# Kernel tuning notes

Measured on AMD Instinct MI355X. Metric: run time of the kernel, lower is better.

## Reference

```python
import jax, jax.numpy as jnp
import numpy as np

B, S, D_MODEL = 2, 2048, 1024
HEADS = 16
DK = D_MODEL // HEADS  # 64
Q_RANK, RANK = 6, 2
ROPE_BASE = 10000.0


def _xavier(key, shape):
    # torch nn.init.xavier_uniform_ on weight (out,in); stored here as (in,out)
    fan_in, fan_out = shape
    a = (6.0 / (fan_in + fan_out)) ** 0.5
    return jax.random.uniform(key, shape, jnp.float32, -a, a)


def setup_inputs() -> dict:
    key = jax.random.key(0)
    ks = jax.random.split(key, 10)
    inp = {
        "q": jax.random.normal(ks[0], (B, S, D_MODEL), jnp.float32),
        "k": jax.random.normal(ks[1], (B, S, D_MODEL), jnp.float32),
        "v": jax.random.normal(ks[2], (B, S, D_MODEL), jnp.float32),
        # causal mask; mask==0 -> -inf in scores
        "mask": jnp.tril(jnp.ones((S, S), dtype=bool))[None, None],
        "W_Aq": _xavier(ks[3], (D_MODEL, Q_RANK * HEADS)),
        "W_Ak": _xavier(ks[4], (D_MODEL, RANK * HEADS)),
        "W_Av": _xavier(ks[5], (D_MODEL, RANK * HEADS)),
        "W_Bq": _xavier(ks[6], (D_MODEL, Q_RANK * DK)),
        "W_Bk": _xavier(ks[7], (D_MODEL, RANK * DK)),
        "W_Bv": _xavier(ks[8], (D_MODEL, RANK * DK)),
        "Wo": _xavier(ks[9], (D_MODEL, D_MODEL)),
    }
    return inp


def _rotary_cos_sin(seq_len, dim):
    inv_freq = 1.0 / (ROPE_BASE ** (jnp.arange(0, dim, 2, dtype=jnp.float32) / dim))
    freqs = jnp.outer(jnp.arange(seq_len, dtype=jnp.float32), inv_freq)  # [S, dim/2]
    return jnp.cos(freqs)[None, :, None, :], jnp.sin(freqs)[None, :, None, :]


def _apply_rotary(x, cos, sin):
    # x: [B, S, R, dk]; rotate-half style RoPE
    d = x.shape[-1] // 2
    x1, x2 = x[..., :d], x[..., d:]
    return jnp.concatenate([x1 * cos + x2 * sin, -x1 * sin + x2 * cos], axis=-1)


def reference(q, k, v, mask, W_Aq, W_Ak, W_Av, W_Bq, W_Bk, W_Bv, Wo):
    Bn, Sn, D = q.shape
    # low-rank factor projections
    A_q = (q @ W_Aq).reshape(Bn, Sn, HEADS, Q_RANK)
    A_k = (k @ W_Ak).reshape(Bn, Sn, HEADS, RANK)
    A_v = (v @ W_Av).reshape(Bn, Sn, HEADS, RANK)
    B_q = (q @ W_Bq).reshape(Bn, Sn, Q_RANK, DK)
    B_k = (k @ W_Bk).reshape(Bn, Sn, RANK, DK)
    B_v = (v @ W_Bv).reshape(Bn, Sn, RANK, DK)
    cos, sin = _rotary_cos_sin(Sn, DK)
    B_q = _apply_rotary(B_q, cos, sin)
    B_k = _apply_rotary(B_k, cos, sin)
    # reconstruct per-head q/k/v: [B,H,S,dk]
    qh = jnp.einsum("bshr,bsrd->bhsd", A_q, B_q) / Q_RANK
    kh = jnp.einsum("bshr,bsrd->bhsd", A_k, B_k) / RANK
    vh = jnp.einsum("bshr,bsrd->bhsd", A_v, B_v) / RANK
    # NOTE: original divides by d_k (not sqrt(d_k)) -- faithful to source
    score = jnp.einsum("bhqd,bhkd->bhqk", qh, kh) / DK
    score = jnp.where(mask, score, -jnp.inf)
    # dropout is identity (eval / dropout=0.0)
    att = jax.nn.softmax(score, axis=-1)
    out = jnp.einsum("bhqk,bhkd->bqhd", att, vh).reshape(Bn, Sn, D)
    return out @ Wo
```

## Files before the change

kernel.cpp:

```cpp
#include <hip/hip_runtime.h>
#include <hip/hip_bf16.h>


typedef __attribute__((ext_vector_type(8))) short short8;
typedef __attribute__((ext_vector_type(4))) float floatx4;

#define MFMA16(a, b, c) __builtin_amdgcn_mfma_f32_16x16x32_bf16(a, b, c, 0, 0, 0)

__device__ __forceinline__ float b2f(short s) {
    unsigned int u = ((unsigned int)(unsigned short)s) << 16;
    float f; __builtin_memcpy(&f, &u, 4); return f;
}
__device__ __forceinline__ unsigned short bfbits(float x) {
    __hip_bfloat16 h = __float2bfloat16(x);
    unsigned short u; __builtin_memcpy(&u, &h, 2); return u;
}

__device__ __forceinline__ float wsrc(int n, int k,
                                      const float* __restrict__ Aq, const float* __restrict__ Bq,
                                      const float* __restrict__ Ak, const float* __restrict__ Bk,
                                      const float* __restrict__ Av, const float* __restrict__ Bv,
                                      const float* __restrict__ Wo) {
    if (n < 96) return Aq[(size_t)k * 96 + n];
    if (n < 480) return Bq[(size_t)k * 384 + (n - 96)];
    if (n < 512) return 0.f;
    if (n < 544) return Ak[(size_t)k * 32 + (n - 512)];
    if (n < 672) return Bk[(size_t)k * 128 + (n - 544)];
    if (n < 768) return 0.f;
    if (n < 800) return Av[(size_t)k * 32 + (n - 768)];
    if (n < 928) return Bv[(size_t)k * 128 + (n - 800)];
    if (n < 1024) return 0.f;
    return Wo[(size_t)k * 1024 + (n - 1024)];
}

__global__ __launch_bounds__(256) void pack_wT_kernel(const float* __restrict__ Aq,
                                                      const float* __restrict__ Bq,
                                                      const float* __restrict__ Ak,
                                                      const float* __restrict__ Bk,
                                                      const float* __restrict__ Av,
                                                      const float* __restrict__ Bv,
                                                      const float* __restrict__ Wo,
                                                      __hip_bfloat16* __restrict__ outBase) {
    __shared__ float tile[64][65];
    int k0 = blockIdx.x * 64, n0 = blockIdx.y * 64;
    int tid = threadIdx.x;
#pragma unroll
    for (int p = 0; p < 16; ++p) {
        int idx = p * 256 + tid;
        int kl = idx >> 6, nl = idx & 63;
        tile[kl][nl] = wsrc(n0 + nl, k0 + kl, Aq, Bq, Ak, Bk, Av, Bv, Wo);
    }
    __syncthreads();
#pragma unroll
    for (int p = 0; p < 16; ++p) {
        int idx = p * 256 + tid;
        int nl = idx >> 6, kl = idx & 63;
        outBase[(size_t)(n0 + nl) * 1024 + k0 + kl] = __float2bfloat16(tile[kl][nl]);
    }
}

__global__ __launch_bounds__(256) void gemm3_kernel(const float* __restrict__ q,
                                                    const float* __restrict__ k,
                                                    const float* __restrict__ v,
                                                    const __hip_bfloat16* __restrict__ WT,
                                                    __hip_bfloat16* __restrict__ Pq,
                                                    __hip_bfloat16* __restrict__ Pk,
                                                    __hip_bfloat16* __restrict__ Pv) {
    __shared__ __align__(16) __hip_bfloat16 As[64][72];
    __shared__ __align__(16) __hip_bfloat16 Bs[128][72];
    int lin = blockIdx.x;
    int t = (lin >> 3) & 7;
    int mi = (lin & 7) + ((lin >> 6) << 3);
    int m0 = mi * 64;
    const float* A; __hip_bfloat16* C; int N, n0, wrow;
    if (t < 4)      { A = q; C = Pq; N = 512; n0 = t * 128;        wrow = t * 128; }
    else if (t < 6) { A = k; C = Pk; N = 256; n0 = (t - 4) * 128;  wrow = 512 + (t - 4) * 128; }
    else            { A = v; C = Pv; N = 256; n0 = (t - 6) * 128;  wrow = 768 + (t - 6) * 128; }
    int tid = threadIdx.x;
    int wave = tid >> 6, lane = tid & 63, quad = lane >> 4, l15 = lane & 15;
    floatx4 acc[4][2];
#pragma unroll
    for (int mt = 0; mt < 4; ++mt)
#pragma unroll
        for (int nt = 0; nt < 2; ++nt) acc[mt][nt] = (floatx4){0.f, 0.f, 0.f, 0.f};

    for (int k0 = 0; k0 < 1024; k0 += 64) {
#pragma unroll
        for (int pp = 0; pp < 4; ++pp) {
            int idx = pp * 256 + tid;
            int row = idx >> 4, c4 = (idx & 15) * 4;
            float4 av = *(const float4*)(A + (size_t)(m0 + row) * 1024 + k0 + c4);
            ushort4 bv;
            bv.x = bfbits(av.x); bv.y = bfbits(av.y); bv.z = bfbits(av.z); bv.w = bfbits(av.w);
            *(ushort4*)&As[row][c4] = bv;
        }
#pragma unroll
        for (int pp = 0; pp < 4; ++pp) {
            int idx = pp * 256 + tid;
            int row = idx >> 3, c8 = (idx & 7) * 8;
            *(uint4*)&Bs[row][c8] = *(const uint4*)(WT + (size_t)(wrow + row) * 1024 + k0 + c8);
        }
        __syncthreads();
#pragma unroll
        for (int ks = 0; ks < 64; ks += 32) {
            short8 af[4], bf[2];
#pragma unroll
            for (int mt = 0; mt < 4; ++mt)
                af[mt] = *(const short8*)&As[mt * 16 + l15][ks + quad * 8];
#pragma unroll
            for (int nt = 0; nt < 2; ++nt)
                bf[nt] = *(const short8*)&Bs[wave * 32 + nt * 16 + l15][ks + quad * 8];
#pragma unroll
            for (int mt = 0; mt < 4; ++mt)
#pragma unroll
                for (int nt = 0; nt < 2; ++nt)
                    acc[mt][nt] = MFMA16(af[mt], bf[nt], acc[mt][nt]);
        }
        __syncthreads();
    }
#pragma unroll
    for (int mt = 0; mt < 4; ++mt)
#pragma unroll
        for (int nt = 0; nt < 2; ++nt)
#pragma unroll
            for (int r = 0; r < 4; ++r) {
                int row = m0 + mt * 16 + quad * 4 + r;
                int col = n0 + wave * 32 + nt * 16 + l15;
                C[(size_t)row * N + col] = __float2bfloat16(acc[mt][nt][r]);
            }
}

__global__ __launch_bounds__(256) void gemm_out_kernel(const __hip_bfloat16* __restrict__ A,
                                                       const __hip_bfloat16* __restrict__ BT,
                                                       float* __restrict__ C) {
    __shared__ __align__(16) __hip_bfloat16 As[64][72];
    __shared__ __align__(16) __hip_bfloat16 Bs[128][72];
    int lin = blockIdx.x;
    int n0 = ((lin >> 3) & 7) * 128;
    int mi = (lin & 7) + ((lin >> 6) << 3);
    int m0 = mi * 64;
    int tid = threadIdx.x;
    int wave = tid >> 6, lane = tid & 63, quad = lane >> 4, l15 = lane & 15;
    floatx4 acc[4][2];
#pragma unroll
    for (int mt = 0; mt < 4; ++mt)
#pragma unroll
        for (int nt = 0; nt < 2; ++nt) acc[mt][nt] = (floatx4){0.f, 0.f, 0.f, 0.f};

    for (int k0 = 0; k0 < 1024; k0 += 64) {
#pragma unroll
        for (int pp = 0; pp < 2; ++pp) {
            int idx = pp * 256 + tid;
            int row = idx >> 3, c8 = (idx & 7) * 8;
            *(uint4*)&As[row][c8] = *(const uint4*)(A + (size_t)(m0 + row) * 1024 + k0 + c8);
        }
#pragma unroll
        for (int pp = 0; pp < 4; ++pp) {
            int idx = pp * 256 + tid;
            int row = idx >> 3, c8 = (idx & 7) * 8;
            *(uint4*)&Bs[row][c8] = *(const uint4*)(BT + (size_t)(n0 + row) * 1024 + k0 + c8);
        }
        __syncthreads();
#pragma unroll
        for (int ks = 0; ks < 64; ks += 32) {
            short8 af[4], bf[2];
#pragma unroll
            for (int mt = 0; mt < 4; ++mt)
                af[mt] = *(const short8*)&As[mt * 16 + l15][ks + quad * 8];
#pragma unroll
            for (int nt = 0; nt < 2; ++nt)
                bf[nt] = *(const short8*)&Bs[wave * 32 + nt * 16 + l15][ks + quad * 8];
#pragma unroll
            for (int mt = 0; mt < 4; ++mt)
#pragma unroll
                for (int nt = 0; nt < 2; ++nt)
                    acc[mt][nt] = MFMA16(af[mt], bf[nt], acc[mt][nt]);
        }
        __syncthreads();
    }
#pragma unroll
    for (int mt = 0; mt < 4; ++mt)
#pragma unroll
        for (int nt = 0; nt < 2; ++nt)
#pragma unroll
            for (int r = 0; r < 4; ++r) {
                int row = m0 + mt * 16 + quad * 4 + r;
                int col = n0 + wave * 32 + nt * 16 + l15;
                C[(size_t)row * 1024 + col] = acc[mt][nt][r];
            }
}

__global__ __launch_bounds__(256) void combine_vt_kernel(const __hip_bfloat16* __restrict__ Pq,
                                                         const __hip_bfloat16* __restrict__ Pk,
                                                         const __hip_bfloat16* __restrict__ Pv,
                                                         __hip_bfloat16* __restrict__ qh,
                                                         __hip_bfloat16* __restrict__ kh,
                                                         __hip_bfloat16* __restrict__ vT) {
    __shared__ __align__(16) __hip_bfloat16 LAq[16][96];
    __shared__ __align__(16) __hip_bfloat16 LAk[16][32];
    __shared__ __align__(16) __hip_bfloat16 LAv[16][32];
    __shared__ __align__(16) __hip_bfloat16 LBq[16][6][72];
    __shared__ __align__(16) __hip_bfloat16 LBk[16][2][72];
    __shared__ __align__(16) __hip_bfloat16 LBv[16][2][72];
    int tid = threadIdx.x;
    int token0 = blockIdx.x * 16;
    int b = token0 >> 11, s0 = token0 & 2047, bh0 = b * 16;

    for (int i = tid; i < 16 * 512; i += 256) {
        int s = i >> 9, c = i & 511;
        __hip_bfloat16 val = Pq[(size_t)(token0 + s) * 512 + c];
        if (c < 96) LAq[s][c] = val;
        else if (c < 480) LBq[s][(c - 96) >> 6][(c - 96) & 63] = val;
    }
    for (int i = tid; i < 16 * 256; i += 256) {
        int s = i >> 8, c = i & 255;
        __hip_bfloat16 vk = Pk[(size_t)(token0 + s) * 256 + c];
        __hip_bfloat16 vv = Pv[(size_t)(token0 + s) * 256 + c];
        if (c < 32) { LAk[s][c] = vk; LAv[s][c] = vv; }
        else if (c < 160) {
            LBk[s][(c - 32) >> 6][(c - 32) & 63] = vk;
            LBv[s][(c - 32) >> 6][(c - 32) & 63] = vv;
        }
    }
    __syncthreads();
    for (int i = tid; i < 4096; i += 256) {
        int s = i >> 8, rr = (i >> 5) & 7, d = i & 31;
        float inv = __expf(-(float)d * 0.28782313662425576f);
        float rev = (float)(s0 + s) * inv * 0.15915494309189535f;
        rev -= floorf(rev);
        float sn = __builtin_amdgcn_sinf(rev);
        float cs = __builtin_amdgcn_cosf(rev);
        if (rr < 6) {
            float x1 = b2f(*(short*)&LBq[s][rr][d]), x2 = b2f(*(short*)&LBq[s][rr][d + 32]);
            LBq[s][rr][d] = __float2bfloat16(x1 * cs + x2 * sn);
            LBq[s][rr][d + 32] = __float2bfloat16(-x1 * sn + x2 * cs);
        } else {
            int r2 = rr - 6;
            float x1 = b2f(*(short*)&LBk[s][r2][d]), x2 = b2f(*(short*)&LBk[s][r2][d + 32]);
            LBk[s][r2][d] = __float2bfloat16(x1 * cs + x2 * sn);
            LBk[s][r2][d + 32] = __float2bfloat16(-x1 * sn + x2 * cs);
        }
    }
    __syncthreads();
    const float QSCALE = 1.4426950408889634f / 768.0f;
    {
        int s = tid >> 4, h = tid & 15;
        float aq[6], ak0, ak1;
#pragma unroll
        for (int r = 0; r < 6; ++r) aq[r] = b2f(*(short*)&LAq[s][h * 6 + r]);
        ak0 = b2f(*(short*)&LAk[s][h * 2]);
        ak1 = b2f(*(short*)&LAk[s][h * 2 + 1]);
        size_t obase = ((size_t)(bh0 + h) * 2048 + s0 + s) * 64;
#pragma unroll
        for (int dc = 0; dc < 64; dc += 8) {
            float accq[8] = {0, 0, 0, 0, 0, 0, 0, 0};
#pragma unroll
            for (int r = 0; r < 6; ++r) {
                short8 bq = *(const short8*)&LBq[s][r][dc];
#pragma unroll
                for (int e = 0; e < 8; ++e) accq[e] += aq[r] * b2f(bq[e]);
            }
            short8 bk0 = *(const short8*)&LBk[s][0][dc];
            short8 bk1 = *(const short8*)&LBk[s][1][dc];
            ushort outq[8], outk[8];
#pragma unroll
            for (int e = 0; e < 8; ++e) {
                outq[e] = bfbits(accq[e] * QSCALE);
                outk[e] = bfbits(ak0 * b2f(bk0[e]) + ak1 * b2f(bk1[e]));
            }
            *(uint4*)((__hip_bfloat16*)qh + obase + dc) = *(uint4*)outq;
            *(uint4*)((__hip_bfloat16*)kh + obase + dc) = *(uint4*)outk;
        }
    }
    {
        int s = tid & 15, dg = tid >> 4;
#pragma unroll
        for (int h = 0; h < 16; ++h) {
            float a0 = b2f(*(short*)&LAv[s][h * 2]) * 0.5f;
            float a1 = b2f(*(short*)&LAv[s][h * 2 + 1]) * 0.5f;
#pragma unroll
            for (int dd = 0; dd < 4; ++dd) {
                int d = dg * 4 + dd;
                float val = a0 * b2f(*(short*)&LBv[s][0][d]) + a1 * b2f(*(short*)&LBv[s][1][d]);
                vT[((size_t)(bh0 + h) * 64 + d) * 2048 + s0 + s] = __float2bfloat16(val);
            }
        }
    }
}

__global__ __launch_bounds__(256) void flash_kernel(const __hip_bfloat16* __restrict__ qh,
                                                    const __hip_bfloat16* __restrict__ kh,
                                                    const __hip_bfloat16* __restrict__ vT,
                                                    __hip_bfloat16* __restrict__ att) {
    int lin = blockIdx.x + (blockIdx.y << 5);
    int bh = ((lin & 7) << 2) | ((lin >> 3) & 3);
    int tpair = lin >> 5;
    int tid = threadIdx.x;
    int wave = tid >> 6, lane = tid & 63, quad = lane >> 4, l15 = lane & 15;
    __shared__ __align__(16) __hip_bfloat16 Ks[64][72];
    __shared__ __align__(16) __hip_bfloat16 Vts[64][72];

    int row0 = tid >> 3, col = (tid & 7) * 8;
    int row1 = 32 + row0;
    const size_t khb = (size_t)bh * 2048 * 64;
    const size_t vtb = (size_t)bh * 64 * 2048;
    uint4 sk0, sk1, sv0, sv1;
#define FL_ISSUE(J)                                                            \
    {                                                                          \
        int k0_ = (J) * 64;                                                    \
        sk0 = *(const uint4*)(kh + khb + (size_t)(k0_ + row0) * 64 + col);     \
        sk1 = *(const uint4*)(kh + khb + (size_t)(k0_ + row1) * 64 + col);     \
        sv0 = *(const uint4*)(vT + vtb + (size_t)row0 * 2048 + k0_ + col);     \
        sv1 = *(const uint4*)(vT + vtb + (size_t)row1 * 2048 + k0_ + col);     \
    }

    for (int pass = 0; pass < 2; ++pass) {
        int qi = pass ? tpair : (31 - tpair);
        int q0 = qi * 64;
        const __hip_bfloat16* qrow =
            qh + ((size_t)bh * 2048 + q0 + wave * 16 + l15) * 64 + quad * 8;
        short8 aq0 = *(const short8*)(qrow);
        short8 aq1 = *(const short8*)(qrow + 32);

        floatx4 o[4];
#pragma unroll
        for (int nt = 0; nt < 4; ++nt) o[nt] = (floatx4){0.f, 0.f, 0.f, 0.f};
        float rs = 0.f;
        int qloc = wave * 16 + l15;

        FL_ISSUE(0);
        for (int j = 0; j <= qi; ++j) {
            __syncthreads();
            *(uint4*)&Ks[row0][col] = sk0;
            *(uint4*)&Ks[row1][col] = sk1;
            *(uint4*)&Vts[row0][col] = sv0;
            *(uint4*)&Vts[row1][col] = sv1;
            __syncthreads();
            if (j < qi) FL_ISSUE(j + 1);

            floatx4 s[4];
#pragma unroll
            for (int nt = 0; nt < 4; ++nt) s[nt] = (floatx4){0.f, 0.f, 0.f, 0.f};
#pragma unroll
            for (int nt = 0; nt < 4; ++nt) {
                short8 bk0 = *(const short8*)&Ks[nt * 16 + l15][quad * 8];
                short8 bk1 = *(const short8*)&Ks[nt * 16 + l15][32 + quad * 8];
                s[nt] = MFMA16(bk0, aq0, s[nt]);
                s[nt] = MFMA16(bk1, aq1, s[nt]);
            }
            if (j == qi) {
#pragma unroll
                for (int nt = 0; nt < 4; ++nt) {
                    int kbase = nt * 16 + quad * 4;
#pragma unroll
                    for (int r = 0; r < 4; ++r)
                        if (kbase + r > qloc) s[nt][r] = -__builtin_inff();
                }
            }
            float pv[4][4];
#pragma unroll
            for (int nt = 0; nt < 4; ++nt)
#pragma unroll
                for (int r = 0; r < 4; ++r) {
                    pv[nt][r] = exp2f(s[nt][r]);
                    rs += pv[nt][r];
                }
            union { ushort u[8]; short8 v; } p0, p1;
#pragma unroll
            for (int r = 0; r < 4; ++r) {
                p0.u[r]     = bfbits(pv[0][r]);
                p0.u[4 + r] = bfbits(pv[1][r]);
                p1.u[r]     = bfbits(pv[2][r]);
                p1.u[4 + r] = bfbits(pv[3][r]);
            }
#pragma unroll
            for (int nt = 0; nt < 4; ++nt) {
                int vr = nt * 16 + l15;
                union { ushort4 h[2]; short8 v; } x0, x1;
                x0.h[0] = *(const ushort4*)&Vts[vr][quad * 4];
                x0.h[1] = *(const ushort4*)&Vts[vr][16 + quad * 4];
                x1.h[0] = *(const ushort4*)&Vts[vr][32 + quad * 4];
                x1.h[1] = *(const ushort4*)&Vts[vr][48 + quad * 4];
                o[nt] = MFMA16(x0.v, p0.v, o[nt]);
                o[nt] = MFMA16(x1.v, p1.v, o[nt]);
            }
        }
        rs += __shfl_xor(rs, 16, 64);
        rs += __shfl_xor(rs, 32, 64);
        float inv = 1.0f / rs;
        int b = bh >> 4, h = bh & 15;
        size_t obase = ((size_t)b * 2048 + q0 + wave * 16 + l15) * 1024 + h * 64 + quad * 4;
#pragma unroll
        for (int nt = 0; nt < 4; ++nt) {
            ushort ow[4];
#pragma unroll
            for (int r = 0; r < 4; ++r) ow[r] = bfbits(o[nt][r] * inv);
            *(ushort4*)((__hip_bfloat16*)att + obase + nt * 16) = *(ushort4*)ow;
        }
    }
#undef FL_ISSUE
}

extern "C" void kernel_launch(void* const* d_in, const int* in_sizes, int n_in,
                              void* d_out, int out_size, void* d_ws, size_t ws_size,
                              hipStream_t stream) {
    const float* q = (const float*)d_in[0];
    const float* k = (const float*)d_in[1];
    const float* v = (const float*)d_in[2];
    const float* W_Aq = (const float*)d_in[4];
    const float* W_Ak = (const float*)d_in[5];
    const float* W_Av = (const float*)d_in[6];
    const float* W_Bq = (const float*)d_in[7];
    const float* W_Bk = (const float*)d_in[8];
    const float* W_Bv = (const float*)d_in[9];
    const float* Wo = (const float*)d_in[10];
    float* out = (float*)d_out;

    char* w = (char*)d_ws;
    __hip_bfloat16* qh  = (__hip_bfloat16*)(w + 0);
    __hip_bfloat16* kh  = (__hip_bfloat16*)(w + 8388608);
    __hip_bfloat16* vT  = (__hip_bfloat16*)(w + 16777216);
    __hip_bfloat16* WT  = (__hip_bfloat16*)(w + 25165824);
    __hip_bfloat16* WoT = WT + (size_t)1024 * 1024;
    __hip_bfloat16* Pq  = (__hip_bfloat16*)(w + 29360128);
    __hip_bfloat16* Pk  = (__hip_bfloat16*)(w + 33554432);
    __hip_bfloat16* Pv  = (__hip_bfloat16*)(w + 35651584);
    __hip_bfloat16* att = (__hip_bfloat16*)(w + 37748736);

    pack_wT_kernel<<<dim3(16, 32), 256, 0, stream>>>(W_Aq, W_Bq, W_Ak, W_Bk, W_Av, W_Bv, Wo, WT);
    gemm3_kernel<<<512, 256, 0, stream>>>(q, k, v, WT, Pq, Pk, Pv);
    combine_vt_kernel<<<256, 256, 0, stream>>>(Pq, Pk, Pv, qh, kh, vT);
    flash_kernel<<<dim3(32, 16), 256, 0, stream>>>(qh, kh, vT, att);
    gemm_out_kernel<<<512, 256, 0, stream>>>(att, WoT, out);
}
```

Measured before the change: 229.9 us.

## Split flash attention KV range across two wave groups with LDS reduction

The flash kernel now runs 512 threads per block. Two groups of four waves each process alternating 64-key tiles from a pair of tiles loaded into double-sized LDS, and the partial outputs and row sums are combined through shared memory at the end. The aim is more waves in flight per Q tile and shorter serial loops over the causal KV range. The cost is an extra LDS reduction and sync per pass, and one group sits idle on the odd final tile.

```diff
diff --git a/kernel.cpp b/kernel.cpp
--- a/kernel.cpp
+++ b/kernel.cpp
@@ -288,7 +288,7 @@
     }
 }
 
-__global__ __launch_bounds__(256) void flash_kernel(const __hip_bfloat16* __restrict__ qh,
+__global__ __launch_bounds__(512) void flash_kernel(const __hip_bfloat16* __restrict__ qh,
                                                     const __hip_bfloat16* __restrict__ kh,
                                                     const __hip_bfloat16* __restrict__ vT,
                                                     __hip_bfloat16* __restrict__ att) {
@@ -297,28 +297,30 @@
     int tpair = lin >> 5;
     int tid = threadIdx.x;
     int wave = tid >> 6, lane = tid & 63, quad = lane >> 4, l15 = lane & 15;
-    __shared__ __align__(16) __hip_bfloat16 Ks[64][72];
-    __shared__ __align__(16) __hip_bfloat16 Vts[64][72];
-
-    int row0 = tid >> 3, col = (tid & 7) * 8;
-    int row1 = 32 + row0;
+    int grp = wave >> 2, wv = wave & 3;
+    __shared__ __align__(16) __hip_bfloat16 Ks[2][64][72];
+    __shared__ __align__(16) __hip_bfloat16 Vts[2][64][72];
+    float* cb = (float*)&Ks[0][0][0];
+
+    int row = tid >> 3, col = (tid & 7) * 8;
     const size_t khb = (size_t)bh * 2048 * 64;
     const size_t vtb = (size_t)bh * 64 * 2048;
     uint4 sk0, sk1, sv0, sv1;
-#define FL_ISSUE(J)                                                            \
-    {                                                                          \
-        int k0_ = (J) * 64;                                                    \
-        sk0 = *(const uint4*)(kh + khb + (size_t)(k0_ + row0) * 64 + col);     \
-        sk1 = *(const uint4*)(kh + khb + (size_t)(k0_ + row1) * 64 + col);     \
-        sv0 = *(const uint4*)(vT + vtb + (size_t)row0 * 2048 + k0_ + col);     \
-        sv1 = *(const uint4*)(vT + vtb + (size_t)row1 * 2048 + k0_ + col);     \
+#define FL_ISSUE(P)                                                                  \
+    {                                                                                \
+        int k0_ = (P) * 128;                                                         \
+        sk0 = *(const uint4*)(kh + khb + (size_t)(k0_ + row) * 64 + col);            \
+        sk1 = *(const uint4*)(kh + khb + (size_t)(k0_ + 64 + row) * 64 + col);       \
+        sv0 = *(const uint4*)(vT + vtb + (size_t)row * 2048 + k0_ + col);            \
+        sv1 = *(const uint4*)(vT + vtb + (size_t)row * 2048 + k0_ + 64 + col);       \
     }
 
     for (int pass = 0; pass < 2; ++pass) {
         int qi = pass ? tpair : (31 - tpair);
         int q0 = qi * 64;
+        int npairs = (qi + 2) >> 1;
         const __hip_bfloat16* qrow =
-            qh + ((size_t)bh * 2048 + q0 + wave * 16 + l15) * 64 + quad * 8;
+            qh + ((size_t)bh * 2048 + q0 + wv * 16 + l15) * 64 + quad * 8;
         short8 aq0 = *(const short8*)(qrow);
         short8 aq1 = *(const short8*)(qrow + 32);
 
@@ -326,76 +328,96 @@
 #pragma unroll
         for (int nt = 0; nt < 4; ++nt) o[nt] = (floatx4){0.f, 0.f, 0.f, 0.f};
         float rs = 0.f;
-        int qloc = wave * 16 + l15;
+        int qloc = wv * 16 + l15;
 
         FL_ISSUE(0);
-        for (int j = 0; j <= qi; ++j) {
+        for (int p = 0; p < npairs; ++p) {
             __syncthreads();
-            *(uint4*)&Ks[row0][col] = sk0;
-            *(uint4*)&Ks[row1][col] = sk1;
-            *(uint4*)&Vts[row0][col] = sv0;
-            *(uint4*)&Vts[row1][col] = sv1;
+            *(uint4*)&Ks[0][row][col] = sk0;
+            *(uint4*)&Ks[1][row][col] = sk1;
+            *(uint4*)&Vts[0][row][col] = sv0;
+            *(uint4*)&Vts[1][row][col] = sv1;
             __syncthreads();
-            if (j < qi) FL_ISSUE(j + 1);
-
-            floatx4 s[4];
-#pragma unroll
-            for (int nt = 0; nt < 4; ++nt) s[nt] = (floatx4){0.f, 0.f, 0.f, 0.f};
+            if (p + 1 < npairs) FL_ISSUE(p + 1);
+
+            int mytile = 2 * p + grp;
+            if (mytile <= qi) {
+                floatx4 s[4];
+#pragma unroll
+                for (int nt = 0; nt < 4; ++nt) s[nt] = (floatx4){0.f, 0.f, 0.f, 0.f};
+#pragma unroll
+                for (int nt = 0; nt < 4; ++nt) {
+                    short8 bk0 = *(const short8*)&Ks[grp][nt * 16 + l15][quad * 8];
+                    short8 bk1 = *(const short8*)&Ks[grp][nt * 16 + l15][32 + quad * 8];
+                    s[nt] = MFMA16(bk0, aq0, s[nt]);
+                    s[nt] = MFMA16(bk1, aq1, s[nt]);
+                }
+                if (mytile == qi) {
+#pragma unroll
+                    for (int nt = 0; nt < 4; ++nt) {
+                        int kbase = nt * 16 + quad * 4;
+#pragma unroll
+                        for (int r = 0; r < 4; ++r)
+                            if (kbase + r > qloc) s[nt][r] = -__builtin_inff();
+                    }
+                }
+                float pv[4][4];
+#pragma unroll
+                for (int nt = 0; nt < 4; ++nt)
+#pragma unroll
+                    for (int r = 0; r < 4; ++r) {
+                        pv[nt][r] = exp2f(s[nt][r]);
+                        rs += pv[nt][r];
+                    }
+                union { ushort u[8]; short8 v; } p0, p1;
+#pragma unroll
+                for (int r = 0; r < 4; ++r) {
+                    p0.u[r]     = bfbits(pv[0][r]);
+                    p0.u[4 + r] = bfbits(pv[1][r]);
+                    p1.u[r]     = bfbits(pv[2][r]);
+                    p1.u[4 + r] = bfbits(pv[3][r]);
+                }
+#pragma unroll
+                for (int nt = 0; nt < 4; ++nt) {
+                    int vr = nt * 16 + l15;
+                    union { ushort4 h[2]; short8 v; } x0, x1;
+                    x0.h[0] = *(const ushort4*)&Vts[grp][vr][quad * 4];
+                    x0.h[1] = *(const ushort4*)&Vts[grp][vr][16 + quad * 4];
+                    x1.h[0] = *(const ushort4*)&Vts[grp][vr][32 + quad * 4];
+                    x1.h[1] = *(const ushort4*)&Vts[grp][vr][48 + quad * 4];
+                    o[nt] = MFMA16(x0.v, p0.v, o[nt]);
+                    o[nt] = MFMA16(x1.v, p1.v, o[nt]);
+                }
+            }
+        }
+        __syncthreads();
+        int cbase = (wv * 64 + lane) * 17;
+        if (grp == 1) {
+#pragma unroll
+            for (int nt = 0; nt < 4; ++nt)
+#pragma unroll
+                for (int r = 0; r < 4; ++r) cb[cbase + nt * 4 + r] = o[nt][r];
+            cb[cbase + 16] = rs;
+        }
+        __syncthreads();
+        if (grp == 0) {
+#pragma unroll
+            for (int nt = 0; nt < 4; ++nt)
+#pragma unroll
+                for (int r = 0; r < 4; ++r) o[nt][r] += cb[cbase + nt * 4 + r];
+            rs += cb[cbase + 16];
+            rs += __shfl_xor(rs, 16, 64);
+            rs += __shfl_xor(rs, 32, 64);
+            float inv = 1.0f / rs;
+            int b = bh >> 4, h = bh & 15;
+            size_t obase = ((size_t)b * 2048 + q0 + wv * 16 + l15) * 1024 + h * 64 + quad * 4;
 #pragma unroll
             for (int nt = 0; nt < 4; ++nt) {
-                short8 bk0 = *(const short8*)&Ks[nt * 16 + l15][quad * 8];
-                short8 bk1 = *(const short8*)&Ks[nt * 16 + l15][32 + quad * 8];
-                s[nt] = MFMA16(bk0, aq0, s[nt]);
-                s[nt] = MFMA16(bk1, aq1, s[nt]);
-            }
-            if (j == qi) {
-#pragma unroll
-                for (int nt = 0; nt < 4; ++nt) {
-                    int kbase = nt * 16 + quad * 4;
-#pragma unroll
-                    for (int r = 0; r < 4; ++r)
-                        if (kbase + r > qloc) s[nt][r] = -__builtin_inff();
-                }
-            }
-            float pv[4][4];
-#pragma unroll
-            for (int nt = 0; nt < 4; ++nt)
-#pragma unroll
-                for (int r = 0; r < 4; ++r) {
-                    pv[nt][r] = exp2f(s[nt][r]);
-                    rs += pv[nt][r];
-                }
-            union { ushort u[8]; short8 v; } p0, p1;
-#pragma unroll
-            for (int r = 0; r < 4; ++r) {
-                p0.u[r]     = bfbits(pv[0][r]);
-                p0.u[4 + r] = bfbits(pv[1][r]);
-                p1.u[r]     = bfbits(pv[2][r]);
-                p1.u[4 + r] = bfbits(pv[3][r]);
-            }
-#pragma unroll
-            for (int nt = 0; nt < 4; ++nt) {
-                int vr = nt * 16 + l15;
-                union { ushort4 h[2]; short8 v; } x0, x1;
-                x0.h[0] = *(const ushort4*)&Vts[vr][quad * 4];
-                x0.h[1] = *(const ushort4*)&Vts[vr][16 + quad * 4];
-                x1.h[0] = *(const ushort4*)&Vts[vr][32 + quad * 4];
-                x1.h[1] = *(const ushort4*)&Vts[vr][48 + quad * 4];
-                o[nt] = MFMA16(x0.v, p0.v, o[nt]);
-                o[nt] = MFMA16(x1.v, p1.v, o[nt]);
-            }
-        }
-        rs += __shfl_xor(rs, 16, 64);
-        rs += __shfl_xor(rs, 32, 64);
-        float inv = 1.0f / rs;
-        int b = bh >> 4, h = bh & 15;
-        size_t obase = ((size_t)b * 2048 + q0 + wave * 16 + l15) * 1024 + h * 64 + quad * 4;
-#pragma unroll
-        for (int nt = 0; nt < 4; ++nt) {
-            ushort ow[4];
-#pragma unroll
-            for (int r = 0; r < 4; ++r) ow[r] = bfbits(o[nt][r] * inv);
-            *(ushort4*)((__hip_bfloat16*)att + obase + nt * 16) = *(ushort4*)ow;
+                ushort ow[4];
+#pragma unroll
+                for (int r = 0; r < 4; ++r) ow[r] = bfbits(o[nt][r] * inv);
+                *(ushort4*)((__hip_bfloat16*)att + obase + nt * 16) = *(ushort4*)ow;
+            }
         }
     }
 #undef FL_ISSUE
@@ -430,6 +452,6 @@
     pack_wT_kernel<<<dim3(16, 32), 256, 0, stream>>>(W_Aq, W_Bq, W_Ak, W_Bk, W_Av, W_Bv, Wo, WT);
     gemm3_kernel<<<512, 256, 0, stream>>>(q, k, v, WT, Pq, Pk, Pv);
     combine_vt_kernel<<<256, 256, 0, stream>>>(Pq, Pk, Pv, qh, kh, vT);
-    flash_kernel<<<dim3(32, 16), 256, 0, stream>>>(qh, kh, vT, att);
+    flash_kernel<<<dim3(32, 16), 512, 0, stream>>>(qh, kh, vT, att);
     gemm_out_kernel<<<512, 256, 0, stream>>>(att, WoT, out);
 }
```

New measurement: 230.0 us. Within noise of the previous version (+0.0%).

## Use 128-row query tiles per block with two 16-row sub-tiles per wave

Applied to the files above, without the earlier changes.

The flash attention kernel now processes one 128-row query tile per block, ordered largest first, instead of two paired 64-row tiles. Each wave handles two 16-row query groups, so every K/V tile staged in shared memory feeds twice as many MFMAs, halving K/V loads and barriers per unit of work. On the final diagonal tile, waves 0–1 skip it because it is fully masked for them. In exchange, register pressure rises, the causal work per block is less evenly balanced, and the block count or occupancy may shift.

```diff
diff --git a/kernel.cpp b/kernel.cpp
--- a/kernel.cpp
+++ b/kernel.cpp
@@ -294,109 +294,133 @@
                                                     __hip_bfloat16* __restrict__ att) {
     int lin = blockIdx.x + (blockIdx.y << 5);
     int bh = ((lin & 7) << 2) | ((lin >> 3) & 3);
-    int tpair = lin >> 5;
+    int t = 15 - (lin >> 5);
     int tid = threadIdx.x;
     int wave = tid >> 6, lane = tid & 63, quad = lane >> 4, l15 = lane & 15;
+    int q0 = t * 128;
+    int ntiles = 2 * t + 2;
     __shared__ __align__(16) __hip_bfloat16 Ks[64][72];
     __shared__ __align__(16) __hip_bfloat16 Vts[64][72];
 
-    int row0 = tid >> 3, col = (tid & 7) * 8;
-    int row1 = 32 + row0;
+    const __hip_bfloat16* qrowA =
+        qh + ((size_t)bh * 2048 + q0 + wave * 32 + l15) * 64 + quad * 8;
+    short8 aqA0 = *(const short8*)(qrowA);
+    short8 aqA1 = *(const short8*)(qrowA + 32);
+    short8 aqB0 = *(const short8*)(qrowA + 16 * 64);
+    short8 aqB1 = *(const short8*)(qrowA + 16 * 64 + 32);
+    int qlocA = wave * 32 + l15;
+    int qlocB = qlocA + 16;
+
+    floatx4 oA[4], oB[4];
+#pragma unroll
+    for (int nt = 0; nt < 4; ++nt) {
+        oA[nt] = (floatx4){0.f, 0.f, 0.f, 0.f};
+        oB[nt] = (floatx4){0.f, 0.f, 0.f, 0.f};
+    }
+    float rsA = 0.f, rsB = 0.f;
+
+    int srow = tid >> 2, sc = (tid & 3) * 8;
     const size_t khb = (size_t)bh * 2048 * 64;
     const size_t vtb = (size_t)bh * 64 * 2048;
     uint4 sk0, sk1, sv0, sv1;
-#define FL_ISSUE(J)                                                            \
-    {                                                                          \
-        int k0_ = (J) * 64;                                                    \
-        sk0 = *(const uint4*)(kh + khb + (size_t)(k0_ + row0) * 64 + col);     \
-        sk1 = *(const uint4*)(kh + khb + (size_t)(k0_ + row1) * 64 + col);     \
-        sv0 = *(const uint4*)(vT + vtb + (size_t)row0 * 2048 + k0_ + col);     \
-        sv1 = *(const uint4*)(vT + vtb + (size_t)row1 * 2048 + k0_ + col);     \
-    }
-
-    for (int pass = 0; pass < 2; ++pass) {
-        int qi = pass ? tpair : (31 - tpair);
-        int q0 = qi * 64;
-        const __hip_bfloat16* qrow =
-            qh + ((size_t)bh * 2048 + q0 + wave * 16 + l15) * 64 + quad * 8;
-        short8 aq0 = *(const short8*)(qrow);
-        short8 aq1 = *(const short8*)(qrow + 32);
-
-        floatx4 o[4];
-#pragma unroll
-        for (int nt = 0; nt < 4; ++nt) o[nt] = (floatx4){0.f, 0.f, 0.f, 0.f};
-        float rs = 0.f;
-        int qloc = wave * 16 + l15;
-
-        FL_ISSUE(0);
-        for (int j = 0; j <= qi; ++j) {
-            __syncthreads();
-            *(uint4*)&Ks[row0][col] = sk0;
-            *(uint4*)&Ks[row1][col] = sk1;
-            *(uint4*)&Vts[row0][col] = sv0;
-            *(uint4*)&Vts[row1][col] = sv1;
-            __syncthreads();
-            if (j < qi) FL_ISSUE(j + 1);
-
-            floatx4 s[4];
-#pragma unroll
-            for (int nt = 0; nt < 4; ++nt) s[nt] = (floatx4){0.f, 0.f, 0.f, 0.f};
+#define FL_ISSUE(J)                                                                \
+    {                                                                              \
+        int k0_ = (J) * 64;                                                        \
+        sk0 = *(const uint4*)(kh + khb + (size_t)(k0_ + srow) * 64 + sc);          \
+        sk1 = *(const uint4*)(kh + khb + (size_t)(k0_ + srow) * 64 + sc + 32);     \
+        sv0 = *(const uint4*)(vT + vtb + (size_t)srow * 2048 + k0_ + sc);          \
+        sv1 = *(const uint4*)(vT + vtb + (size_t)srow * 2048 + k0_ + sc + 32);     \
+    }
+
+    FL_ISSUE(0);
+    for (int j = 0; j < ntiles; ++j) {
+        __syncthreads();
+        *(uint4*)&Ks[srow][sc] = sk0;
+        *(uint4*)&Ks[srow][sc + 32] = sk1;
+        *(uint4*)&Vts[srow][sc] = sv0;
+        *(uint4*)&Vts[srow][sc + 32] = sv1;
+        __syncthreads();
+        if (j + 1 < ntiles) FL_ISSUE(j + 1);
+
+        int krel0 = (j - 2 * t) * 64;
+        if (krel0 == 64 && wave < 2) continue;
+
+        floatx4 sA[4], sB[4];
+#pragma unroll
+        for (int nt = 0; nt < 4; ++nt) {
+            sA[nt] = (floatx4){0.f, 0.f, 0.f, 0.f};
+            sB[nt] = (floatx4){0.f, 0.f, 0.f, 0.f};
+        }
+#pragma unroll
+        for (int nt = 0; nt < 4; ++nt) {
+            short8 bk0 = *(const short8*)&Ks[nt * 16 + l15][quad * 8];
+            short8 bk1 = *(const short8*)&Ks[nt * 16 + l15][32 + quad * 8];
+            sA[nt] = MFMA16(bk0, aqA0, sA[nt]);
+            sA[nt] = MFMA16(bk1, aqA1, sA[nt]);
+            sB[nt] = MFMA16(bk0, aqB0, sB[nt]);
+            sB[nt] = MFMA16(bk1, aqB1, sB[nt]);
+        }
+        if (krel0 >= 0) {
 #pragma unroll
             for (int nt = 0; nt < 4; ++nt) {
-                short8 bk0 = *(const short8*)&Ks[nt * 16 + l15][quad * 8];
-                short8 bk1 = *(const short8*)&Ks[nt * 16 + l15][32 + quad * 8];
-                s[nt] = MFMA16(bk0, aq0, s[nt]);
-                s[nt] = MFMA16(bk1, aq1, s[nt]);
-            }
-            if (j == qi) {
-#pragma unroll
-                for (int nt = 0; nt < 4; ++nt) {
-                    int kbase = nt * 16 + quad * 4;
-#pragma unroll
-                    for (int r = 0; r < 4; ++r)
-                        if (kbase + r > qloc) s[nt][r] = -__builtin_inff();
+                int kb = krel0 + nt * 16 + quad * 4;
+#pragma unroll
+                for (int r = 0; r < 4; ++r) {
+                    if (kb + r > qlocA) sA[nt][r] = -__builtin_inff();
+                    if (kb + r > qlocB) sB[nt][r] = -__builtin_inff();
                 }
             }
-            float pv[4][4];
-#pragma unroll
-            for (int nt = 0; nt < 4; ++nt)
-#pragma unroll
-                for (int r = 0; r < 4; ++r) {
-                    pv[nt][r] = exp2f(s[nt][r]);
-                    rs += pv[nt][r];
-                }
-            union { ushort u[8]; short8 v; } p0, p1;
+        }
+        float pvA[4][4], pvB[4][4];
+#pragma unroll
+        for (int nt = 0; nt < 4; ++nt)
 #pragma unroll
             for (int r = 0; r < 4; ++r) {
-                p0.u[r]     = bfbits(pv[0][r]);
-                p0.u[4 + r] = bfbits(pv[1][r]);
-                p1.u[r]     = bfbits(pv[2][r]);
-                p1.u[4 + r] = bfbits(pv[3][r]);
-            }
-#pragma unroll
-            for (int nt = 0; nt < 4; ++nt) {
-                int vr = nt * 16 + l15;
-                union { ushort4 h[2]; short8 v; } x0, x1;
-                x0.h[0] = *(const ushort4*)&Vts[vr][quad * 4];
-                x0.h[1] = *(const ushort4*)&Vts[vr][16 + quad * 4];
-                x1.h[0] = *(const ushort4*)&Vts[vr][32 + quad * 4];
-                x1.h[1] = *(const ushort4*)&Vts[vr][48 + quad * 4];
-                o[nt] = MFMA16(x0.v, p0.v, o[nt]);
-                o[nt] = MFMA16(x1.v, p1.v, o[nt]);
-            }
-        }
-        rs += __shfl_xor(rs, 16, 64);
-        rs += __shfl_xor(rs, 32, 64);
-        float inv = 1.0f / rs;
-        int b = bh >> 4, h = bh & 15;
-        size_t obase = ((size_t)b * 2048 + q0 + wave * 16 + l15) * 1024 + h * 64 + quad * 4;
+                pvA[nt][r] = exp2f(sA[nt][r]);
+                rsA += pvA[nt][r];
+                pvB[nt][r] = exp2f(sB[nt][r]);
+                rsB += pvB[nt][r];
+            }
+        union { ushort u[8]; short8 v; } pA0, pA1, pB0, pB1;
+#pragma unroll
+        for (int r = 0; r < 4; ++r) {
+            pA0.u[r] = bfbits(pvA[0][r]); pA0.u[4 + r] = bfbits(pvA[1][r]);
+            pA1.u[r] = bfbits(pvA[2][r]); pA1.u[4 + r] = bfbits(pvA[3][r]);
+            pB0.u[r] = bfbits(pvB[0][r]); pB0.u[4 + r] = bfbits(pvB[1][r]);
+            pB1.u[r] = bfbits(pvB[2][r]); pB1.u[4 + r] = bfbits(pvB[3][r]);
+        }
 #pragma unroll
         for (int nt = 0; nt < 4; ++nt) {
-            ushort ow[4];
-#pragma unroll
-            for (int r = 0; r < 4; ++r) ow[r] = bfbits(o[nt][r] * inv);
-            *(ushort4*)((__hip_bfloat16*)att + obase + nt * 16) = *(ushort4*)ow;
-        }
+            int vr = nt * 16 + l15;
+            union { ushort4 h[2]; short8 v; } x0, x1;
+            x0.h[0] = *(const ushort4*)&Vts[vr][quad * 4];
+            x0.h[1] = *(const ushort4*)&Vts[vr][16 + quad * 4];
+            x1.h[0] = *(const ushort4*)&Vts[vr][32 + quad * 4];
+            x1.h[1] = *(const ushort4*)&Vts[vr][48 + quad * 4];
+            oA[nt] = MFMA16(x0.v, pA0.v, oA[nt]);
+            oA[nt] = MFMA16(x1.v, pA1.v, oA[nt]);
+            oB[nt] = MFMA16(x0.v, pB0.v, oB[nt]);
+            oB[nt] = MFMA16(x1.v, pB1.v, oB[nt]);
+        }
+    }
+    rsA += __shfl_xor(rsA, 16, 64);
+    rsA += __shfl_xor(rsA, 32, 64);
+    rsB += __shfl_xor(rsB, 16, 64);
+    rsB += __shfl_xor(rsB, 32, 64);
+    float invA = 1.0f / rsA, invB = 1.0f / rsB;
+    int b = bh >> 4, h = bh & 15;
+    size_t obA = ((size_t)b * 2048 + q0 + wave * 32 + l15) * 1024 + h * 64 + quad * 4;
+    size_t obB = obA + (size_t)16 * 1024;
+#pragma unroll
+    for (int nt = 0; nt < 4; ++nt) {
+        ushort owA[4], owB[4];
+#pragma unroll
+        for (int r = 0; r < 4; ++r) {
+            owA[r] = bfbits(oA[nt][r] * invA);
+            owB[r] = bfbits(oB[nt][r] * invB);
+        }
+        *(ushort4*)((__hip_bfloat16*)att + obA + nt * 16) = *(ushort4*)owA;
+        *(ushort4*)((__hip_bfloat16*)att + obB + nt * 16) = *(ushort4*)owB;
     }
 #undef FL_ISSUE
 }
```

Result: slower. 240.8 us (+4.7%).
